# Optimization experiments

Hardware: AMD Instinct MI355X
Metric: run time of the kernel (lower is better)

## Reference

```python
import jax, jax.numpy as jnp
import numpy as np

B, S, D = 8, 2048, 512
EPS = 1e-6
ROPE_THETA = 10000.0


def setup_inputs() -> dict:
    key = jax.random.key(0)
    ks = jax.random.split(key, 8)
    scale = 0.02
    return {
        "x": jax.random.normal(ks[0], (B, S, D), dtype=jnp.float32),
        "conv_w": jax.random.normal(ks[1], (D, D, 3), dtype=jnp.float32) * scale,
        "conv_b": jnp.zeros((D,), dtype=jnp.float32),
        "pre_g": jnp.ones((D,), dtype=jnp.float32),
        "q_g": jnp.ones((D,), dtype=jnp.float32),
        "k_g": jnp.ones((D,), dtype=jnp.float32),
        "Wq": jax.random.normal(ks[2], (D, D), dtype=jnp.float32) * scale,
        "Wk": jax.random.normal(ks[3], (D, D), dtype=jnp.float32) * scale,
        "Wv": jax.random.normal(ks[4], (D, D), dtype=jnp.float32) * scale,
    }


def _rmsnorm(x, g, eps=EPS):
    ms = jnp.mean(jnp.square(x), axis=-1, keepdims=True)
    return x * jax.lax.rsqrt(ms + eps) * g


def _rope_tables(seq_len, head_dim, dtype=jnp.float32):
    inv = 1.0 / (ROPE_THETA ** (jnp.arange(0, head_dim, 2, dtype=dtype) / head_dim))
    freqs = jnp.arange(seq_len, dtype=dtype)[:, None] * inv[None, :]  # [S, D/2]
    return jnp.cos(freqs), jnp.sin(freqs)


def _apply_rope(x, cos, sin):
    # x: [B, S, D]; treat last dim as D/2 complex pairs (interleaved real/imag)
    b, s, d = x.shape
    xr = x.reshape(b, s, d // 2, 2)
    x0, x1 = xr[..., 0], xr[..., 1]
    c = cos[None, :, :]
    sn = sin[None, :, :]
    o0 = x0 * c - x1 * sn
    o1 = x0 * sn + x1 * c
    return jnp.stack([o0, o1], axis=-1).reshape(b, s, d)


def reference(x, conv_w, conv_b, pre_g, q_g, k_g, Wq, Wk, Wv):
    b, s, d = x.shape
    # Conv1d over sequence axis (kernel 3, padding 1)
    xc = jnp.transpose(x, (0, 2, 1))  # [B, D, S]
    xc = jax.lax.conv_general_dilated(
        xc, conv_w, window_strides=(1,), padding=[(1, 1)],
        dimension_numbers=("NCH", "OIH", "NCH"))
    xc = xc + conv_b[None, :, None]
    x_norm = _rmsnorm(jnp.transpose(xc, (0, 2, 1)), pre_g)  # [B, S, D]

    q = _rmsnorm(jnp.einsum("bsd,ed->bse", x_norm, Wq), q_g)
    k = _rmsnorm(jnp.einsum("bsd,ed->bse", x_norm, Wk), k_g)
    v = jnp.einsum("bsd,ed->bse", x_norm, Wv)

    cos, sin = _rope_tables(s, d, x.dtype)
    q = _apply_rope(q, cos, sin)
    k = _apply_rope(k, cos, sin)

    scores = jnp.einsum("bqd,bkd->bqk", q, k) / jnp.sqrt(jnp.asarray(d, x.dtype))
    w = jax.nn.softmax(scores, axis=-1)  # dropout is identity in eval mode
    attended = jnp.einsum("bqk,bkd->bqd", w, v)
    out = x + attended
    return out.mean(axis=1)  # [B, D]
```

## Files before the change

### kernel.cpp

```cpp
#include <hip/hip_runtime.h>
#include <math.h>

#define BB 8
#define SS 2048
#define SSG 2050
#define DDIM 512
#define KC 1536
#define EPSV 1e-6f
#define SCALE 0.044194173824159216f

typedef unsigned short ushort_t;
using short8 = __attribute__((ext_vector_type(8))) short;
using f32x4  = __attribute__((ext_vector_type(4))) float;

__device__ inline unsigned short f2bf(float f) {
    union { float f; unsigned int u; } v; v.f = f;
    unsigned int r = v.u + 0x7FFFu + ((v.u >> 16) & 1u);
    return (unsigned short)(r >> 16);
}
__device__ inline unsigned int packbf(float a, float b) {
    return (unsigned int)f2bf(a) | ((unsigned int)f2bf(b) << 16);
}
__device__ inline float bf2f(unsigned short s) {
    union { unsigned int u; float f; } v; v.u = ((unsigned int)s) << 16; return v.f;
}

__device__ inline void gload16(const ushort_t* g, ushort_t* l) {
    __builtin_amdgcn_global_load_lds(
        (__attribute__((address_space(1))) const void*)g,
        (__attribute__((address_space(3))) void*)l, 16, 0, 0);
}

__device__ inline short8 ldswz(const ushort_t* s, int row, int c) {
    return *reinterpret_cast<const short8*>(&s[(row << 6) + ((c ^ (row & 7)) << 3)]);
}

__global__ __launch_bounds__(256) void kx_cast(const float* __restrict__ x,
                                               ushort_t* __restrict__ xbf,
                                               float* __restrict__ xsum)
{
    const int t = threadIdx.x;
    const int b = blockIdx.x;
    const int r0 = blockIdx.y * 16;
    const int c0 = 2 * t;
    if (blockIdx.y == 0) {
        *reinterpret_cast<unsigned int*>(&xbf[((size_t)b * SSG) * DDIM + c0]) = 0u;
        *reinterpret_cast<unsigned int*>(&xbf[((size_t)b * SSG + SS + 1) * DDIM + c0]) = 0u;
    }
    float s0 = 0.f, s1 = 0.f;
    for (int r = 0; r < 16; r++) {
        size_t srow = (size_t)b * SS + r0 + r;
        size_t drow = (size_t)b * SSG + 1 + r0 + r;
        float2 v = *reinterpret_cast<const float2*>(&x[srow * DDIM + c0]);
        s0 += v.x; s1 += v.y;
        *reinterpret_cast<unsigned int*>(&xbf[drow * DDIM + c0]) = packbf(v.x, v.y);
    }
    atomicAdd(&xsum[b * DDIM + c0], s0);
    atomicAdd(&xsum[b * DDIM + c0 + 1], s1);
}

__global__ __launch_bounds__(256) void k0_prep(
    const float* __restrict__ conv_w, const float* __restrict__ Wq,
    const float* __restrict__ Wk, const float* __restrict__ Wv,
    const float* __restrict__ pre_g,
    ushort_t* __restrict__ wcat, ushort_t* __restrict__ wqkv,
    float* __restrict__ rope)
{
    int idx = blockIdx.x * 256 + threadIdx.x;
    {
        int o = idx / KC, kk = idx - o * KC;
        int t = kk >> 9, i = kk & 511;
        wcat[idx] = f2bf(conv_w[(size_t)o * KC + i * 3 + t]);
    }
    {
        int n = idx >> 9, d = idx & 511;
        const float* src = (n < 512) ? &Wq[(size_t)n * DDIM + d]
                         : (n < 1024) ? &Wk[(size_t)(n - 512) * DDIM + d]
                         : &Wv[(size_t)(n - 1024) * DDIM + d];
        wqkv[idx] = f2bf(*src * pre_g[d]);
    }
    if (blockIdx.x < SS / 8) {
        const int t = threadIdx.x;
        const int r0 = blockIdx.x * 8;
        const float invf = (float)pow(10000.0, -(double)(2 * t) / (double)DDIM);
        for (int r = 0; r < 8; r++) {
            int srow = r0 + r;
            float sn, cs;
            sincosf((float)srow * invf, &sn, &cs);
            *reinterpret_cast<float2*>(&rope[((size_t)srow << 9) + 2 * t]) = make_float2(cs, sn);
        }
    }
}

#define COMPUTE_TILE(Acur, Bcur) do { \
    _Pragma("unroll") \
    for (int half = 0; half < 2; half++) { \
        const int cb = (half << 2) | lq; \
        short8 af0 = ldswz(Acur, wm * 64 +  0 + lm, cb); \
        short8 af1 = ldswz(Acur, wm * 64 + 16 + lm, cb); \
        short8 af2 = ldswz(Acur, wm * 64 + 32 + lm, cb); \
        short8 af3 = ldswz(Acur, wm * 64 + 48 + lm, cb); \
        _Pragma("unroll") \
        for (int nt = 0; nt < 4; nt++) { \
            short8 bfv = ldswz(Bcur, wn * 64 + nt * 16 + lm, cb); \
            acc[0][nt] = __builtin_amdgcn_mfma_f32_16x16x32_bf16(af0, bfv, acc[0][nt], 0, 0, 0); \
            acc[1][nt] = __builtin_amdgcn_mfma_f32_16x16x32_bf16(af1, bfv, acc[1][nt], 0, 0, 0); \
            acc[2][nt] = __builtin_amdgcn_mfma_f32_16x16x32_bf16(af2, bfv, acc[2][nt], 0, 0, 0); \
            acc[3][nt] = __builtin_amdgcn_mfma_f32_16x16x32_bf16(af3, bfv, acc[3][nt], 0, 0, 0); \
        } \
    } } while (0)

__global__ __launch_bounds__(256) void k1b_conv(
    const ushort_t* __restrict__ xbf, const ushort_t* __restrict__ wcat,
    const float* __restrict__ conv_b, ushort_t* __restrict__ ybf, float* __restrict__ rs)
{
    __shared__ alignas(16) ushort_t As[128 * 64];
    __shared__ alignas(16) ushort_t Bs[128 * 64];
    const int t = threadIdx.x;
    const int lane = t & 63, w = t >> 6;
    const int lm = lane & 15, lq = lane >> 4;
    const int wm = w >> 1, wn = w & 1;
    const int lr = lane >> 3;
    const int lc = ((lane & 7) ^ lr) << 3;
    const int b  = blockIdx.x;
    const int s0 = blockIdx.y * 128;
    const int n0 = blockIdx.z * 128;
    const ushort_t* Ag = xbf + (size_t)b * SSG * DDIM;
    const ushort_t* Bg = wcat + (size_t)n0 * KC;

    const ushort_t* pa[4]; const ushort_t* pb[4];
    int la[4];
    #pragma unroll
    for (int i = 0; i < 4; i++) {
        const int tr = (w * 4 + i) * 8 + lr;
        pa[i] = &Ag[(size_t)(s0 + tr) * DDIM + lc];
        pb[i] = &Bg[(size_t)tr * KC + lc];
        la[i] = (w * 4 + i) * 512;
    }

    f32x4 acc[4][4];
    #pragma unroll
    for (int i = 0; i < 4; i++)
        #pragma unroll
        for (int j = 0; j < 4; j++) acc[i][j] = (f32x4){0.f, 0.f, 0.f, 0.f};

    for (int dc = 0; dc < 24; dc++) {
        __syncthreads();
        const int koff = dc * 64;
        #pragma unroll
        for (int i = 0; i < 4; i++) {
            gload16(pa[i] + koff, &As[la[i]]);
            gload16(pb[i] + koff, &Bs[la[i]]);
        }
        __syncthreads();
        COMPUTE_TILE(As, Bs);
    }

    const int rbase = s0 + wm * 64;
    const int cbase = n0 + wn * 64;
    ushort_t* yb = ybf + (size_t)b * SS * DDIM;
    float* rsb = rs + (size_t)b * SS;
    float bias[4];
    #pragma unroll
    for (int nt = 0; nt < 4; nt++) bias[nt] = conv_b[cbase + nt * 16 + lm];
    #pragma unroll
    for (int mt = 0; mt < 4; mt++) {
        float pr[4] = {0.f, 0.f, 0.f, 0.f};
        #pragma unroll
        for (int nt = 0; nt < 4; nt++) {
            #pragma unroll
            for (int r = 0; r < 4; r++) {
                float val = acc[mt][nt][r] + bias[nt];
                yb[(size_t)(rbase + mt * 16 + lq * 4 + r) * DDIM + cbase + nt * 16 + lm] = f2bf(val);
                pr[r] = fmaf(val, val, pr[r]);
            }
        }
        #pragma unroll
        for (int r = 0; r < 4; r++) {
            float p = pr[r];
            p += __shfl_xor(p, 1, 64); p += __shfl_xor(p, 2, 64);
            p += __shfl_xor(p, 4, 64); p += __shfl_xor(p, 8, 64);
            if (lm == 0) atomicAdd(&rsb[rbase + mt * 16 + lq * 4 + r], p);
        }
    }
}

__global__ __launch_bounds__(256) void k1c_qkv(
    const ushort_t* __restrict__ ybf, const float* __restrict__ rs,
    const ushort_t* __restrict__ wqkv,
    ushort_t* __restrict__ qraw, ushort_t* __restrict__ kraw, ushort_t* __restrict__ vb,
    float* __restrict__ rq, float* __restrict__ rk)
{
    __shared__ alignas(16) ushort_t As[128 * 64];
    __shared__ alignas(16) ushort_t Bs[128 * 64];
    const int t = threadIdx.x;
    const int lane = t & 63, w = t >> 6;
    const int lm = lane & 15, lq = lane >> 4;
    const int wm = w >> 1, wn = w & 1;
    const int lr = lane >> 3;
    const int lc = ((lane & 7) ^ lr) << 3;
    const int b  = blockIdx.x;
    const int s0 = blockIdx.y * 128;
    const int nt9 = blockIdx.z;
    const int n0 = nt9 * 128;
    const ushort_t* Ag = ybf + ((size_t)b * SS + s0) * DDIM;
    const ushort_t* Bg = wqkv + (size_t)n0 * DDIM;

    const ushort_t* pa[4]; const ushort_t* pb[4];
    int la[4];
    #pragma unroll
    for (int i = 0; i < 4; i++) {
        const int tr = (w * 4 + i) * 8 + lr;
        pa[i] = &Ag[(size_t)tr * DDIM + lc];
        pb[i] = &Bg[(size_t)tr * DDIM + lc];
        la[i] = (w * 4 + i) * 512;
    }

    f32x4 acc[4][4];
    #pragma unroll
    for (int i = 0; i < 4; i++)
        #pragma unroll
        for (int j = 0; j < 4; j++) acc[i][j] = (f32x4){0.f, 0.f, 0.f, 0.f};

    for (int dc = 0; dc < 8; dc++) {
        __syncthreads();
        const int koff = dc * 64;
        #pragma unroll
        for (int i = 0; i < 4; i++) {
            gload16(pa[i] + koff, &As[la[i]]);
            gload16(pb[i] + koff, &Bs[la[i]]);
        }
        __syncthreads();
        COMPUTE_TILE(As, Bs);
    }

    const int which = nt9 >> 2;
    const int rbase = s0 + wm * 64;
    const int cbase = ((nt9 & 3) * 128) + wn * 64;
    const float* rsb = rs + (size_t)b * SS;
    float inv[4][4];
    #pragma unroll
    for (int mt = 0; mt < 4; mt++)
        #pragma unroll
        for (int r = 0; r < 4; r++)
            inv[mt][r] = rsqrtf(rsb[rbase + mt * 16 + lq * 4 + r] * (1.0f / DDIM) + EPSV);

    if (which == 2) {
        ushort_t* vbb = vb + (size_t)b * SS * DDIM;
        #pragma unroll
        for (int mt = 0; mt < 4; mt++)
            #pragma unroll
            for (int nt = 0; nt < 4; nt++)
                #pragma unroll
                for (int r = 0; r < 4; r++)
                    vbb[(size_t)(rbase + mt * 16 + lq * 4 + r) * DDIM + cbase + nt * 16 + lm] =
                        f2bf(acc[mt][nt][r] * inv[mt][r]);
    } else {
        ushort_t* db2 = (which ? kraw : qraw) + (size_t)b * SS * DDIM;
        float* rb = (which ? rk : rq) + (size_t)b * SS;
        #pragma unroll
        for (int mt = 0; mt < 4; mt++) {
            float pr[4] = {0.f, 0.f, 0.f, 0.f};
            #pragma unroll
            for (int nt = 0; nt < 4; nt++) {
                #pragma unroll
                for (int r = 0; r < 4; r++) {
                    float val = acc[mt][nt][r] * inv[mt][r];
                    db2[(size_t)(rbase + mt * 16 + lq * 4 + r) * DDIM + cbase + nt * 16 + lm] = f2bf(val);
                    pr[r] = fmaf(val, val, pr[r]);
                }
            }
            #pragma unroll
            for (int r = 0; r < 4; r++) {
                float p = pr[r];
                p += __shfl_xor(p, 1, 64); p += __shfl_xor(p, 2, 64);
                p += __shfl_xor(p, 4, 64); p += __shfl_xor(p, 8, 64);
                if (lm == 0) atomicAdd(&rb[rbase + mt * 16 + lq * 4 + r], p);
            }
        }
    }
}

__global__ __launch_bounds__(256) void k1d_rope(
    ushort_t* q_io, ushort_t* k_io,
    const float* __restrict__ rq, const float* __restrict__ rk,
    const float* __restrict__ q_g, const float* __restrict__ k_g,
    const float* __restrict__ rope)
{
    const int t = threadIdx.x;
    const int b = blockIdx.x;
    const int r0 = blockIdx.y * 8;
    const int tr = t >> 6;
    const int c0 = (t & 63) * 8;
    float4 qg0 = *reinterpret_cast<const float4*>(&q_g[c0]);
    float4 qg1 = *reinterpret_cast<const float4*>(&q_g[c0 + 4]);
    float4 kg0 = *reinterpret_cast<const float4*>(&k_g[c0]);
    float4 kg1 = *reinterpret_cast<const float4*>(&k_g[c0 + 4]);
    const float qg[8] = {qg0.x, qg0.y, qg0.z, qg0.w, qg1.x, qg1.y, qg1.z, qg1.w};
    const float kg[8] = {kg0.x, kg0.y, kg0.z, kg0.w, kg1.x, kg1.y, kg1.z, kg1.w};
    #pragma unroll
    for (int r = 0; r < 2; r++) {
        const int srow = r0 + tr + 4 * r;
        const size_t rowi = (size_t)b * SS + srow;
        const float iq = rsqrtf(rq[rowi] * (1.0f / DDIM) + EPSV);
        const float ik = rsqrtf(rk[rowi] * (1.0f / DDIM) + EPSV);
        const size_t off = rowi * DDIM + c0;
        uint4 qv = *reinterpret_cast<const uint4*>(&q_io[off]);
        uint4 kv = *reinterpret_cast<const uint4*>(&k_io[off]);
        float4 cs0 = *reinterpret_cast<const float4*>(&rope[((size_t)srow << 9) + c0]);
        float4 cs1 = *reinterpret_cast<const float4*>(&rope[((size_t)srow << 9) + c0 + 4]);
        const float cs[4] = {cs0.x, cs0.z, cs1.x, cs1.z};
        const float sn[4] = {cs0.y, cs0.w, cs1.y, cs1.w};
        unsigned int qw[4] = {qv.x, qv.y, qv.z, qv.w};
        unsigned int kw[4] = {kv.x, kv.y, kv.z, kv.w};
        uint4 qo, ko;
        unsigned int* qop = &qo.x; unsigned int* kop = &ko.x;
        #pragma unroll
        for (int j = 0; j < 4; j++) {
            float qa = bf2f((ushort_t)(qw[j] & 0xFFFF)) * iq * qg[2 * j];
            float qb = bf2f((ushort_t)(qw[j] >> 16))    * iq * qg[2 * j + 1];
            float ka = bf2f((ushort_t)(kw[j] & 0xFFFF)) * ik * kg[2 * j];
            float kb = bf2f((ushort_t)(kw[j] >> 16))    * ik * kg[2 * j + 1];
            qop[j] = packbf(qa * cs[j] - qb * sn[j], qa * sn[j] + qb * cs[j]);
            kop[j] = packbf(ka * cs[j] - kb * sn[j], ka * sn[j] + kb * cs[j]);
        }
        *reinterpret_cast<uint4*>(&q_io[off]) = qo;
        *reinterpret_cast<uint4*>(&k_io[off]) = ko;
    }
}

__global__ __launch_bounds__(256) void k2a_rowsum(
    const ushort_t* __restrict__ qb, const ushort_t* __restrict__ kb,
    ushort_t* __restrict__ P, float* __restrict__ l)
{
    __shared__ alignas(16) ushort_t As[128 * 64];
    __shared__ alignas(16) ushort_t Bs[128 * 64];
    const int t = threadIdx.x;
    const int lane = t & 63, w = t >> 6;
    const int lm = lane & 15, lq = lane >> 4;
    const int wm = w >> 1, wn = w & 1;
    const int lr = lane >> 3;
    const int lc = ((lane & 7) ^ lr) << 3;
    const int b  = blockIdx.x;
    const int qt = blockIdx.y;
    const int kt = blockIdx.z;
    const ushort_t* Ag = qb + ((size_t)b * SS + qt * 128) * DDIM;
    const ushort_t* Bg = kb + ((size_t)b * SS + kt * 128) * DDIM;

    const ushort_t* pa[4]; const ushort_t* pb[4];
    int la[4];
    #pragma unroll
    for (int i = 0; i < 4; i++) {
        const int tr = (w * 4 + i) * 8 + lr;
        pa[i] = &Ag[(size_t)tr * DDIM + lc];
        pb[i] = &Bg[(size_t)tr * DDIM + lc];
        la[i] = (w * 4 + i) * 512;
    }

    f32x4 acc[4][4];
    #pragma unroll
    for (int i = 0; i < 4; i++)
        #pragma unroll
        for (int j = 0; j < 4; j++) acc[i][j] = (f32x4){0.f, 0.f, 0.f, 0.f};

    for (int dc = 0; dc < 8; dc++) {
        __syncthreads();
        const int koff = dc * 64;
        #pragma unroll
        for (int i = 0; i < 4; i++) {
            gload16(pa[i] + koff, &As[la[i]]);
            gload16(pb[i] + koff, &Bs[la[i]]);
        }
        __syncthreads();
        COMPUTE_TILE(As, Bs);
    }

    const int rbase = qt * 128 + wm * 64;
    const int cbase = kt * 128 + wn * 64;
    ushort_t* Pb = P + (size_t)b * SS * SS;
    float* lrow = l + (size_t)b * SS;
    #pragma unroll
    for (int mt = 0; mt < 4; mt++) {
        #pragma unroll
        for (int r = 0; r < 4; r++) {
            const int row = rbase + mt * 16 + lq * 4 + r;
            float rowp = 0.f;
            #pragma unroll
            for (int nt = 0; nt < 4; nt++) {
                float e = __expf(acc[mt][nt][r] * SCALE);
                Pb[(size_t)row * SS + cbase + nt * 16 + lm] = f2bf(e);
                rowp += e;
            }
            float p = rowp;
            p += __shfl_xor(p, 1, 64); p += __shfl_xor(p, 2, 64);
            p += __shfl_xor(p, 4, 64); p += __shfl_xor(p, 8, 64);
            if (lm == 0) atomicAdd(&lrow[row], p);
        }
    }
}

__global__ __launch_bounds__(256) void k2c_colred(
    const ushort_t* __restrict__ P, const float* __restrict__ l,
    float* __restrict__ cw)
{
    const int t = threadIdx.x;
    const int b = blockIdx.x;
    const int q0 = blockIdx.y * 128;
    const int k0 = blockIdx.z * 1024 + t * 4;
    const ushort_t* Pb = P + ((size_t)b * SS + q0) * SS;
    const float* lb = l + (size_t)b * SS + q0;
    float a0 = 0.f, a1 = 0.f, a2 = 0.f, a3 = 0.f;
    for (int q = 0; q < 128; q++) {
        float rl = 1.0f / lb[q];
        uint2 pp = *reinterpret_cast<const uint2*>(&Pb[(size_t)q * SS + k0]);
        a0 = fmaf(bf2f((ushort_t)(pp.x & 0xFFFF)), rl, a0);
        a1 = fmaf(bf2f((ushort_t)(pp.x >> 16)), rl, a1);
        a2 = fmaf(bf2f((ushort_t)(pp.y & 0xFFFF)), rl, a2);
        a3 = fmaf(bf2f((ushort_t)(pp.y >> 16)), rl, a3);
    }
    atomicAdd(&cw[(size_t)b * SS + k0], a0);
    atomicAdd(&cw[(size_t)b * SS + k0 + 1], a1);
    atomicAdd(&cw[(size_t)b * SS + k0 + 2], a2);
    atomicAdd(&cw[(size_t)b * SS + k0 + 3], a3);
}

__global__ __launch_bounds__(256) void k4_out(
    const float* __restrict__ xsum, const ushort_t* __restrict__ v,
    const float* __restrict__ cwv, float* __restrict__ out)
{
    const int b = blockIdx.x, c = blockIdx.y;
    const int t = threadIdx.x;
    const int srow0 = c * (SS / 16);
    const ushort_t* vb = v + ((size_t)b * SS + srow0) * DDIM;
    const float* cwb   = cwv + (size_t)b * SS + srow0;
    float a0 = (c == 0) ? xsum[b * DDIM + t]       : 0.f;
    float a1 = (c == 0) ? xsum[b * DDIM + t + 256] : 0.f;
    for (int r = 0; r < SS / 16; r++) {
        float w = cwb[r];
        a0 += w * bf2f(vb[(size_t)r * DDIM + t]);
        a1 += w * bf2f(vb[(size_t)r * DDIM + t + 256]);
    }
    atomicAdd(&out[b * DDIM + t],       a0 * (1.0f / SS));
    atomicAdd(&out[b * DDIM + t + 256], a1 * (1.0f / SS));
}

extern "C" void kernel_launch(void* const* d_in, const int* in_sizes, int n_in,
                              void* d_out, int out_size, void* d_ws, size_t ws_size,
                              hipStream_t stream)
{
    const float* x      = (const float*)d_in[0];
    const float* conv_w = (const float*)d_in[1];
    const float* conv_b = (const float*)d_in[2];
    const float* pre_g  = (const float*)d_in[3];
    const float* q_g    = (const float*)d_in[4];
    const float* k_g    = (const float*)d_in[5];
    const float* Wq     = (const float*)d_in[6];
    const float* Wk     = (const float*)d_in[7];
    const float* Wv     = (const float*)d_in[8];
    float* out          = (float*)d_out;

    const size_t NTOK  = (size_t)BB * SS * DDIM;
    const size_t NTOKG = (size_t)BB * SSG * DDIM;
    char* p = (char*)d_ws;
    ushort_t* xbf = (ushort_t*)p; p += NTOKG * 2;
    ushort_t* ybf = (ushort_t*)p; p += NTOK * 2;
     p += NTOK * 2;
    char* padreg = p;             p += NTOK * 2;
    ushort_t* qio = (ushort_t*)p; p += NTOK * 2;
    ushort_t* kio = (ushort_t*)p; p += NTOK * 2;
    ushort_t* vb  = (ushort_t*)p; p += NTOK * 2;
    ushort_t* wcat = (ushort_t*)p; p += (size_t)DDIM * KC * 2;
    ushort_t* wqkv = (ushort_t*)p; p += (size_t)KC * DDIM * 2;
    float* rs   = (float*)p; p += (size_t)BB * SS * 4;
    float* rq   = (float*)p; p += (size_t)BB * SS * 4;
    float* rk   = (float*)p; p += (size_t)BB * SS * 4;
    float* lbuf = (float*)p; p += (size_t)BB * SS * 4;
    float* cwb  = (float*)p; p += (size_t)BB * SS * 4;
    float* xsum = (float*)p; p += (size_t)BB * DDIM * 4;

    ushort_t* Pbuf = xbf;
    float* rope = (float*)padreg;

    (void)hipMemsetAsync(d_out, 0, (size_t)out_size * sizeof(float), stream);
    (void)hipMemsetAsync(rs, 0, ((size_t)BB * SS * 5 + (size_t)BB * DDIM) * sizeof(float), stream);

    kx_cast<<<dim3(BB, SS / 16), 256, 0, stream>>>(x, xbf, xsum);
    k0_prep<<<dim3(DDIM * KC / 256), 256, 0, stream>>>(conv_w, Wq, Wk, Wv, pre_g, wcat, wqkv, rope);
    k1b_conv<<<dim3(BB, SS / 128, 4), 256, 0, stream>>>(xbf, wcat, conv_b, ybf, rs);
    k1c_qkv<<<dim3(BB, SS / 128, 12), 256, 0, stream>>>(ybf, rs, wqkv, qio, kio, vb, rq, rk);
    k1d_rope<<<dim3(BB, SS / 8), 256, 0, stream>>>(qio, kio, rq, rk, q_g, k_g, rope);
    k2a_rowsum<<<dim3(BB, SS / 128, SS / 128), 256, 0, stream>>>(qio, kio, Pbuf, lbuf);
    k2c_colred<<<dim3(BB, SS / 128, SS / 1024), 256, 0, stream>>>(Pbuf, lbuf, cwb);
    k4_out<<<dim3(BB, 16), 256, 0, stream>>>(xsum, vb, cwb, out);
}
```

Baseline: 267.0 us.

## Use 256x128 tiles with 512 threads and triple-buffered LDS ring in GEMMs

Rewrites the three MFMA GEMM kernels (conv, QKV, QK^T) to use 512-thread blocks covering 256x128 output tiles. Each kernel now runs a three-stage LDS ring with async global-to-LDS loads issued two k-steps ahead, waiting on a vmcnt count instead of double __syncthreads. The aim is to overlap global loads with MFMA compute and to reuse each B tile across more rows. In exchange it uses about 144KB of LDS, which limits each CU to one block, and halves the grid size.

```diff
diff --git a/kernel.cpp b/kernel.cpp
--- a/kernel.cpp
+++ b/kernel.cpp
@@ -110,33 +110,49 @@
         } \
     } } while (0)
 
-__global__ __launch_bounds__(256) void k1b_conv(
+#define STAGE_RING(ktn) do { \
+    const int _ko = (ktn) * 64; \
+    ushort_t* _sa = &As[(ktn) % 3][(w * 8) * 64]; \
+    ushort_t* _sb = &Bs[(ktn) % 3][(w * 8) * 64]; \
+    gload16(pA + _ko,                          _sa); \
+    gload16(pA + (size_t)64  * DDIM + _ko,     _sa + 64 * 64); \
+    gload16(pA + (size_t)128 * DDIM + _ko,     _sa + 128 * 64); \
+    gload16(pA + (size_t)192 * DDIM + _ko,     _sa + 192 * 64); \
+    gload16(pB + _ko,                          _sb); \
+    gload16(pB + (size_t)64 * bpitch + _ko,    _sb + 64 * 64); \
+} while (0)
+
+#define GEMM_RING_LOOP(NT) \
+    STAGE_RING(0); STAGE_RING(1); \
+    for (int kt = 0; kt < (NT); ++kt) { \
+        if (kt == (NT) - 1) asm volatile("s_waitcnt vmcnt(0)\n\ts_barrier" ::: "memory"); \
+        else                asm volatile("s_waitcnt vmcnt(6)\n\ts_barrier" ::: "memory"); \
+        if (kt + 2 < (NT)) STAGE_RING(kt + 2); \
+        const ushort_t* Ac = &As[kt % 3][0]; \
+        const ushort_t* Bc = &Bs[kt % 3][0]; \
+        COMPUTE_TILE(Ac, Bc); \
+    }
+
+__global__ __launch_bounds__(512, 1) void k1b_conv(
     const ushort_t* __restrict__ xbf, const ushort_t* __restrict__ wcat,
     const float* __restrict__ conv_b, ushort_t* __restrict__ ybf, float* __restrict__ rs)
 {
-    __shared__ alignas(16) ushort_t As[128 * 64];
-    __shared__ alignas(16) ushort_t Bs[128 * 64];
+    __shared__ alignas(16) ushort_t As[3][256 * 64];
+    __shared__ alignas(16) ushort_t Bs[3][128 * 64];
     const int t = threadIdx.x;
     const int lane = t & 63, w = t >> 6;
     const int lm = lane & 15, lq = lane >> 4;
     const int wm = w >> 1, wn = w & 1;
-    const int lr = lane >> 3;
-    const int lc = ((lane & 7) ^ lr) << 3;
     const int b  = blockIdx.x;
-    const int s0 = blockIdx.y * 128;
+    const int s0 = blockIdx.y * 256;
     const int n0 = blockIdx.z * 128;
     const ushort_t* Ag = xbf + (size_t)b * SSG * DDIM;
     const ushort_t* Bg = wcat + (size_t)n0 * KC;
-
-    const ushort_t* pa[4]; const ushort_t* pb[4];
-    int la[4];
-    #pragma unroll
-    for (int i = 0; i < 4; i++) {
-        const int tr = (w * 4 + i) * 8 + lr;
-        pa[i] = &Ag[(size_t)(s0 + tr) * DDIM + lc];
-        pb[i] = &Bg[(size_t)tr * KC + lc];
-        la[i] = (w * 4 + i) * 512;
-    }
+    const int bpitch = KC;
+    const int srow = w * 8 + (lane >> 3);
+    const int schk = ((lane & 7) ^ (lane >> 3)) << 3;
+    const ushort_t* pA = Ag + (size_t)(s0 + srow) * DDIM + schk;
+    const ushort_t* pB = Bg + (size_t)srow * bpitch + schk;
 
     f32x4 acc[4][4];
     #pragma unroll
@@ -144,17 +160,7 @@
         #pragma unroll
         for (int j = 0; j < 4; j++) acc[i][j] = (f32x4){0.f, 0.f, 0.f, 0.f};
 
-    for (int dc = 0; dc < 24; dc++) {
-        __syncthreads();
-        const int koff = dc * 64;
-        #pragma unroll
-        for (int i = 0; i < 4; i++) {
-            gload16(pa[i] + koff, &As[la[i]]);
-            gload16(pb[i] + koff, &Bs[la[i]]);
-        }
-        __syncthreads();
-        COMPUTE_TILE(As, Bs);
-    }
+    GEMM_RING_LOOP(24);
 
     const int rbase = s0 + wm * 64;
     const int cbase = n0 + wn * 64;
@@ -185,36 +191,28 @@
     }
 }
 
-__global__ __launch_bounds__(256) void k1c_qkv(
+__global__ __launch_bounds__(512, 1) void k1c_qkv(
     const ushort_t* __restrict__ ybf, const float* __restrict__ rs,
     const ushort_t* __restrict__ wqkv,
     ushort_t* __restrict__ qraw, ushort_t* __restrict__ kraw, ushort_t* __restrict__ vb,
     float* __restrict__ rq, float* __restrict__ rk)
 {
-    __shared__ alignas(16) ushort_t As[128 * 64];
-    __shared__ alignas(16) ushort_t Bs[128 * 64];
+    __shared__ alignas(16) ushort_t As[3][256 * 64];
+    __shared__ alignas(16) ushort_t Bs[3][128 * 64];
     const int t = threadIdx.x;
     const int lane = t & 63, w = t >> 6;
     const int lm = lane & 15, lq = lane >> 4;
     const int wm = w >> 1, wn = w & 1;
-    const int lr = lane >> 3;
-    const int lc = ((lane & 7) ^ lr) << 3;
     const int b  = blockIdx.x;
-    const int s0 = blockIdx.y * 128;
+    const int s0 = blockIdx.y * 256;
     const int nt9 = blockIdx.z;
-    const int n0 = nt9 * 128;
     const ushort_t* Ag = ybf + ((size_t)b * SS + s0) * DDIM;
-    const ushort_t* Bg = wqkv + (size_t)n0 * DDIM;
-
-    const ushort_t* pa[4]; const ushort_t* pb[4];
-    int la[4];
-    #pragma unroll
-    for (int i = 0; i < 4; i++) {
-        const int tr = (w * 4 + i) * 8 + lr;
-        pa[i] = &Ag[(size_t)tr * DDIM + lc];
-        pb[i] = &Bg[(size_t)tr * DDIM + lc];
-        la[i] = (w * 4 + i) * 512;
-    }
+    const ushort_t* Bg = wqkv + (size_t)nt9 * 128 * DDIM;
+    const int bpitch = DDIM;
+    const int srow = w * 8 + (lane >> 3);
+    const int schk = ((lane & 7) ^ (lane >> 3)) << 3;
+    const ushort_t* pA = Ag + (size_t)srow * DDIM + schk;
+    const ushort_t* pB = Bg + (size_t)srow * bpitch + schk;
 
     f32x4 acc[4][4];
     #pragma unroll
@@ -222,17 +220,7 @@
         #pragma unroll
         for (int j = 0; j < 4; j++) acc[i][j] = (f32x4){0.f, 0.f, 0.f, 0.f};
 
-    for (int dc = 0; dc < 8; dc++) {
-        __syncthreads();
-        const int koff = dc * 64;
-        #pragma unroll
-        for (int i = 0; i < 4; i++) {
-            gload16(pa[i] + koff, &As[la[i]]);
-            gload16(pb[i] + koff, &Bs[la[i]]);
-        }
-        __syncthreads();
-        COMPUTE_TILE(As, Bs);
-    }
+    GEMM_RING_LOOP(8);
 
     const int which = nt9 >> 2;
     const int rbase = s0 + wm * 64;
@@ -329,33 +317,26 @@
     }
 }
 
-__global__ __launch_bounds__(256) void k2a_rowsum(
+__global__ __launch_bounds__(512, 1) void k2a_rowsum(
     const ushort_t* __restrict__ qb, const ushort_t* __restrict__ kb,
     ushort_t* __restrict__ P, float* __restrict__ l)
 {
-    __shared__ alignas(16) ushort_t As[128 * 64];
-    __shared__ alignas(16) ushort_t Bs[128 * 64];
+    __shared__ alignas(16) ushort_t As[3][256 * 64];
+    __shared__ alignas(16) ushort_t Bs[3][128 * 64];
     const int t = threadIdx.x;
     const int lane = t & 63, w = t >> 6;
     const int lm = lane & 15, lq = lane >> 4;
     const int wm = w >> 1, wn = w & 1;
-    const int lr = lane >> 3;
-    const int lc = ((lane & 7) ^ lr) << 3;
-    const int b  = blockIdx.x;
-    const int qt = blockIdx.y;
-    const int kt = blockIdx.z;
-    const ushort_t* Ag = qb + ((size_t)b * SS + qt * 128) * DDIM;
-    const ushort_t* Bg = kb + ((size_t)b * SS + kt * 128) * DDIM;
-
-    const ushort_t* pa[4]; const ushort_t* pb[4];
-    int la[4];
-    #pragma unroll
-    for (int i = 0; i < 4; i++) {
-        const int tr = (w * 4 + i) * 8 + lr;
-        pa[i] = &Ag[(size_t)tr * DDIM + lc];
-        pb[i] = &Bg[(size_t)tr * DDIM + lc];
-        la[i] = (w * 4 + i) * 512;
-    }
+    const int b   = blockIdx.x;
+    const int qt  = blockIdx.y;
+    const int ktb = blockIdx.z;
+    const ushort_t* Ag = qb + ((size_t)b * SS + qt * 256) * DDIM;
+    const ushort_t* Bg = kb + ((size_t)b * SS + ktb * 128) * DDIM;
+    const int bpitch = DDIM;
+    const int srow = w * 8 + (lane >> 3);
+    const int schk = ((lane & 7) ^ (lane >> 3)) << 3;
+    const ushort_t* pA = Ag + (size_t)srow * DDIM + schk;
+    const ushort_t* pB = Bg + (size_t)srow * bpitch + schk;
 
     f32x4 acc[4][4];
     #pragma unroll
@@ -363,20 +344,10 @@
         #pragma unroll
         for (int j = 0; j < 4; j++) acc[i][j] = (f32x4){0.f, 0.f, 0.f, 0.f};
 
-    for (int dc = 0; dc < 8; dc++) {
-        __syncthreads();
-        const int koff = dc * 64;
-        #pragma unroll
-        for (int i = 0; i < 4; i++) {
-            gload16(pa[i] + koff, &As[la[i]]);
-            gload16(pb[i] + koff, &Bs[la[i]]);
-        }
-        __syncthreads();
-        COMPUTE_TILE(As, Bs);
-    }
-
-    const int rbase = qt * 128 + wm * 64;
-    const int cbase = kt * 128 + wn * 64;
+    GEMM_RING_LOOP(8);
+
+    const int rbase = qt * 256 + wm * 64;
+    const int cbase = ktb * 128 + wn * 64;
     ushort_t* Pb = P + (size_t)b * SS * SS;
     float* lrow = l + (size_t)b * SS;
     #pragma unroll
@@ -464,7 +435,7 @@
     char* p = (char*)d_ws;
     ushort_t* xbf = (ushort_t*)p; p += NTOKG * 2;
     ushort_t* ybf = (ushort_t*)p; p += NTOK * 2;
-     p += NTOK * 2;
+                 p += NTOK * 2;
     char* padreg = p;             p += NTOK * 2;
     ushort_t* qio = (ushort_t*)p; p += NTOK * 2;
     ushort_t* kio = (ushort_t*)p; p += NTOK * 2;
@@ -486,10 +457,10 @@
 
     kx_cast<<<dim3(BB, SS / 16), 256, 0, stream>>>(x, xbf, xsum);
     k0_prep<<<dim3(DDIM * KC / 256), 256, 0, stream>>>(conv_w, Wq, Wk, Wv, pre_g, wcat, wqkv, rope);
-    k1b_conv<<<dim3(BB, SS / 128, 4), 256, 0, stream>>>(xbf, wcat, conv_b, ybf, rs);
-    k1c_qkv<<<dim3(BB, SS / 128, 12), 256, 0, stream>>>(ybf, rs, wqkv, qio, kio, vb, rq, rk);
+    k1b_conv<<<dim3(BB, SS / 256, 4), 512, 0, stream>>>(xbf, wcat, conv_b, ybf, rs);
+    k1c_qkv<<<dim3(BB, SS / 256, 12), 512, 0, stream>>>(ybf, rs, wqkv, qio, kio, vb, rq, rk);
     k1d_rope<<<dim3(BB, SS / 8), 256, 0, stream>>>(qio, kio, rq, rk, q_g, k_g, rope);
-    k2a_rowsum<<<dim3(BB, SS / 128, SS / 128), 256, 0, stream>>>(qio, kio, Pbuf, lbuf);
+    k2a_rowsum<<<dim3(BB, SS / 256, SS / 128), 512, 0, stream>>>(qio, kio, Pbuf, lbuf);
     k2c_colred<<<dim3(BB, SS / 128, SS / 1024), 256, 0, stream>>>(Pbuf, lbuf, cwb);
     k4_out<<<dim3(BB, 16), 256, 0, stream>>>(xsum, vb, cwb, out);
 }
```

New measurement: 278.4 us. 1.04x slower.
